# Kernel optimization log

Hardware: AMD Instinct MI355X
Metric: run time of the kernel (lower is better)

Reference implementation:

```python
import jax, jax.numpy as jnp
import numpy as np

EMB = 768
HEADS = 8
HEAD_DIM = EMB // HEADS  # 96
SCALING = HEAD_DIM ** -0.5


def setup_inputs() -> dict:
    key = jax.random.key(0)
    ks = jax.random.split(key, 9)
    B, S = 2, 2048
    std = 1.0 / np.sqrt(EMB)
    x = jax.random.normal(ks[0], (B, S, EMB), dtype=jnp.float32)
    # torch nn.Linear weights are [out, in]; we store [in, out] for x @ W.
    Wq = jax.random.normal(ks[1], (EMB, EMB), dtype=jnp.float32) * std
    Wk = jax.random.normal(ks[2], (EMB, EMB), dtype=jnp.float32) * std
    Wv = jax.random.normal(ks[3], (EMB, EMB), dtype=jnp.float32) * std
    Wo = jax.random.normal(ks[4], (EMB, EMB), dtype=jnp.float32) * std
    bq = jax.random.normal(ks[5], (EMB,), dtype=jnp.float32) * std
    bk = jax.random.normal(ks[6], (EMB,), dtype=jnp.float32) * std
    bv = jax.random.normal(ks[7], (EMB,), dtype=jnp.float32) * std
    bo = jax.random.normal(ks[8], (EMB,), dtype=jnp.float32) * std
    return {"x": x, "Wq": Wq, "bq": bq, "Wk": Wk, "bk": bk,
            "Wv": Wv, "bv": bv, "Wo": Wo, "bo": bo}


def _split_heads(t):
    # [B, S, E] -> [B, H, S, D]
    B, S, _ = t.shape
    return t.reshape(B, S, HEADS, HEAD_DIM).transpose(0, 2, 1, 3)


def reference(x, Wq, bq, Wk, bk, Wv, bv, Wo, bo):
    q = _split_heads(x @ Wq + bq)
    k = _split_heads(x @ Wk + bk)
    v = _split_heads(x @ Wv + bv)
    # Full [B, H, S, S] score matrix, as in the source module.
    energies = jnp.einsum('bhqd,bhkd->bhqk', q, k)
    # Faithful quirk: softmax first, THEN multiply by scaling (dropout=0 -> identity).
    attention = jax.nn.softmax(energies, axis=-1) * SCALING
    out = jnp.einsum('bhqk,bhkd->bhqd', attention, v)
    B, H, S, D = out.shape
    out = out.transpose(0, 2, 1, 3).reshape(B, S, H * D)
    return out @ Wo + bo
```

## Files before the change

### kernel.cpp

```cpp
#include <hip/hip_runtime.h>
#include <hip/hip_bf16.h>

#define EMB 768
#define HD 96
#define NH 8
#define SEQ 2048
#define SCALING 0.10206207261596575f

typedef short bf16x8 __attribute__((ext_vector_type(8)));
typedef float f32x4  __attribute__((ext_vector_type(4)));
typedef unsigned short u16v8 __attribute__((ext_vector_type(8)));
typedef unsigned short u16v4 __attribute__((ext_vector_type(4)));

union F4 { float4 v; float f[4]; };

__device__ __forceinline__ unsigned short f2bf(float v) {
    __hip_bfloat16 b = __float2bfloat16(v);
    return *reinterpret_cast<unsigned short*>(&b);
}
__device__ __forceinline__ float bf2f(unsigned short u) {
    __hip_bfloat16 b = *reinterpret_cast<__hip_bfloat16*>(&u);
    return __bfloat162float(b);
}

__device__ __forceinline__ void dma16(const unsigned short* g, unsigned short* l) {
    __builtin_amdgcn_global_load_lds(
        (const __attribute__((address_space(1))) unsigned int*)g,
        (__attribute__((address_space(3))) unsigned int*)l,
        16, 0, 0);
}

__global__ __launch_bounds__(256) void convert_x(
    const float* __restrict__ x,
    unsigned short* __restrict__ xh, unsigned short* __restrict__ xl)
{
    const size_t i0 = ((size_t)blockIdx.x * 256 + threadIdx.x) * 8;
    F4 a, b;
    a.v = *(const float4*)&x[i0];
    b.v = *(const float4*)&x[i0 + 4];
    u16v8 h, l;
    #pragma unroll
    for (int j = 0; j < 4; j++) {
        unsigned short hu = f2bf(a.f[j]);
        h[j] = hu; l[j] = f2bf(a.f[j] - bf2f(hu));
    }
    #pragma unroll
    for (int j = 0; j < 4; j++) {
        unsigned short hu = f2bf(b.f[j]);
        h[4+j] = hu; l[4+j] = f2bf(b.f[j] - bf2f(hu));
    }
    *(u16v8*)&xh[i0] = h;
    *(u16v8*)&xl[i0] = l;
}

__global__ __launch_bounds__(256) void convert_wT(
    const float* __restrict__ Wq, const float* __restrict__ Wk,
    const float* __restrict__ Wv, const float* __restrict__ Wo,
    unsigned short* __restrict__ WhT, unsigned short* __restrict__ WlT)
{
    const int z = blockIdx.z;
    const float* W = (z == 0) ? Wq : (z == 1) ? Wk : (z == 2) ? Wv : Wo;
    unsigned short* oh = WhT + (size_t)z * 589824;
    unsigned short* ol = WlT + (size_t)z * 589824;
    __shared__ float T[64][68];
    const int t = threadIdx.x;
    const int r = t >> 2, cg = (t & 3) * 16;
    const int k0 = blockIdx.x * 64, n0 = blockIdx.y * 64;
    #pragma unroll
    for (int i = 0; i < 4; i++) {
        float4 v = *(const float4*)&W[(size_t)(k0 + r) * EMB + n0 + cg + 4*i];
        *(float4*)&T[r][cg + 4*i] = v;
    }
    __syncthreads();
    #pragma unroll
    for (int i = 0; i < 4; i++) {
        u16v4 h, l;
        #pragma unroll
        for (int j = 0; j < 4; j++) {
            float v = T[cg + 4*i + j][r];
            unsigned short hu = f2bf(v);
            h[j] = hu; l[j] = f2bf(v - bf2f(hu));
        }
        *(u16v4*)&oh[(size_t)(n0 + r) * EMB + k0 + cg + 4*i] = h;
        *(u16v4*)&ol[(size_t)(n0 + r) * EMB + k0 + cg + 4*i] = l;
    }
}

#define QA_H 0
#define QA_L 4096
#define QW_H 8192
#define QW_L 12288

__global__ __launch_bounds__(256, 3) void qkv_mfma(
    const unsigned short* __restrict__ xh, const unsigned short* __restrict__ xl,
    const unsigned short* __restrict__ WhT, const unsigned short* __restrict__ WlT,
    const float* __restrict__ bq, const float* __restrict__ bk, const float* __restrict__ bv,
    unsigned short* __restrict__ Qh, unsigned short* __restrict__ Ql,
    unsigned short* __restrict__ Kb, unsigned short* __restrict__ Vt)
{
    const int which = blockIdx.z;
    const unsigned short* Wh = WhT + (size_t)which * 589824;
    const unsigned short* Wl = WlT + (size_t)which * 589824;
    const float* bias = (which == 0) ? bq : (which == 1) ? bk : bv;

    __shared__ __align__(16) unsigned short lds[16384];
    const int tid = threadIdx.x;
    const int lane = tid & 63, lo = lane & 15, h4 = lane >> 4;
    const int w = tid >> 6, wm = w & 1, wn = w >> 1;
    const int row0 = blockIdx.x * 128, col0 = blockIdx.y * 128;

    const unsigned short* sbase =
        (w == 0) ? xh + (size_t)row0 * EMB :
        (w == 1) ? xl + (size_t)row0 * EMB :
        (w == 2) ? Wh + (size_t)col0 * EMB :
                   Wl + (size_t)col0 * EMB;
    const int soff = w * 4096;

    f32x4 acc[4][4];
    #pragma unroll
    for (int i = 0; i < 4; i++)
        #pragma unroll
        for (int j = 0; j < 4; j++) acc[i][j] = (f32x4){0.f, 0.f, 0.f, 0.f};

    for (int k0 = 0; k0 < EMB; k0 += 32) {
        #pragma unroll
        for (int j = 0; j < 8; j++) {
            const int u = j*64 + lane;
            const int row = u >> 2, c8 = (u & 3) * 8;
            dma16(sbase + (size_t)row * EMB + k0 + c8, &lds[soff + j*512]);
        }
        __syncthreads();

        bf16x8 ah[4], al[4];
        #pragma unroll
        for (int i = 0; i < 4; i++)
            ah[i] = *(const bf16x8*)&lds[QA_H + (64*wm + 16*i + lo)*32 + 8*h4];
        if (which <= 1) {
            #pragma unroll
            for (int i = 0; i < 4; i++)
                al[i] = *(const bf16x8*)&lds[QA_L + (64*wm + 16*i + lo)*32 + 8*h4];
        }
        #pragma unroll
        for (int j = 0; j < 4; j++) {
            bf16x8 whf = *(const bf16x8*)&lds[QW_H + (64*wn + 16*j + lo)*32 + 8*h4];
            #pragma unroll
            for (int i = 0; i < 4; i++)
                acc[i][j] = __builtin_amdgcn_mfma_f32_16x16x32_bf16(ah[i], whf, acc[i][j], 0, 0, 0);
            if (which <= 1) {
                #pragma unroll
                for (int i = 0; i < 4; i++)
                    acc[i][j] = __builtin_amdgcn_mfma_f32_16x16x32_bf16(al[i], whf, acc[i][j], 0, 0, 0);
            }
            if (which != 1) {
                bf16x8 wlf = *(const bf16x8*)&lds[QW_L + (64*wn + 16*j + lo)*32 + 8*h4];
                #pragma unroll
                for (int i = 0; i < 4; i++)
                    acc[i][j] = __builtin_amdgcn_mfma_f32_16x16x32_bf16(ah[i], wlf, acc[i][j], 0, 0, 0);
            }
        }
        __syncthreads();
    }

    if (which == 0) {
        #pragma unroll
        for (int i = 0; i < 4; i++)
            #pragma unroll
            for (int r = 0; r < 4; r++) {
                const int sg = row0 + 64*wm + 16*i + 4*h4 + r;
                const int b = sg >> 11, s = sg & 2047;
                #pragma unroll
                for (int j = 0; j < 4; j++) {
                    const int c = col0 + 64*wn + 16*j + lo;
                    const int h = c / HD, d = c - h*HD;
                    float v = acc[i][j][r] + bias[c];
                    unsigned short hu = f2bf(v);
                    const size_t base = ((size_t)(b*NH + h) * SEQ + s) * HD + d;
                    Qh[base] = hu;
                    Ql[base] = f2bf(v - bf2f(hu));
                }
            }
    } else if (which == 1) {
        #pragma unroll
        for (int i = 0; i < 4; i++)
            #pragma unroll
            for (int r = 0; r < 4; r++) {
                const int sg = row0 + 64*wm + 16*i + 4*h4 + r;
                const int b = sg >> 11, s = sg & 2047;
                #pragma unroll
                for (int j = 0; j < 4; j++) {
                    const int c = col0 + 64*wn + 16*j + lo;
                    const int h = c / HD, d = c - h*HD;
                    float v = acc[i][j][r] + bias[c];
                    Kb[((size_t)(b*NH + h) * SEQ + s) * HD + d] = f2bf(v);
                }
            }
    } else {
        #pragma unroll
        for (int i = 0; i < 4; i++)
            #pragma unroll
            for (int r = 0; r < 4; r++) {
                const int sg = row0 + 64*wm + 16*i + 4*h4 + r;
                const int b = sg >> 11, s = sg & 2047;
                #pragma unroll
                for (int j = 0; j < 4; j++) {
                    const int c = col0 + 64*wn + 16*j + lo;
                    const int h = c / HD, d = c - h*HD;
                    float v = acc[i][j][r] + bias[c];
                    Vt[((size_t)(b*NH + h) * HD + d) * SEQ + s] = f2bf(v);
                }
            }
    }
}

#define PA_O 0
#define PWH_O 4096
#define PWL_O 6144

__global__ __launch_bounds__(256, 3) void proj_mfma(
    const unsigned short* __restrict__ AOh,
    const unsigned short* __restrict__ Wh, const unsigned short* __restrict__ Wl,
    const float* __restrict__ bo, float* __restrict__ out)
{
    __shared__ __align__(16) unsigned short lds[8192];
    const int tid = threadIdx.x;
    const int lane = tid & 63, lo = lane & 15, h4 = lane >> 4;
    const int w = tid >> 6, wm = w & 1, wn = w >> 1;
    const int row0 = blockIdx.x * 128, col0 = blockIdx.y * 64;

    const unsigned short* sbase =
        (w <= 1) ? AOh + (size_t)row0 * EMB :
        (w == 2) ? Wh  + (size_t)col0 * EMB :
                   Wl  + (size_t)col0 * EMB;
    const int jbase = (w == 1) ? 4 : 0;
    const int soff  = (w <= 1) ? PA_O : (w == 2) ? PWH_O : PWL_O;

    f32x4 acc[4][2];
    #pragma unroll
    for (int i = 0; i < 4; i++)
        #pragma unroll
        for (int j = 0; j < 2; j++) acc[i][j] = (f32x4){0.f, 0.f, 0.f, 0.f};

    for (int k0 = 0; k0 < EMB; k0 += 32) {
        #pragma unroll
        for (int jj = 0; jj < 4; jj++) {
            const int j = jbase + jj;
            const int u = j*64 + lane;
            const int row = u >> 2, c8 = (u & 3) * 8;
            dma16(sbase + (size_t)row * EMB + k0 + c8, &lds[soff + j*512]);
        }
        __syncthreads();

        bf16x8 af[4];
        #pragma unroll
        for (int i = 0; i < 4; i++)
            af[i] = *(const bf16x8*)&lds[PA_O + (64*wm + 16*i + lo)*32 + 8*h4];
        #pragma unroll
        for (int j = 0; j < 2; j++) {
            bf16x8 whf = *(const bf16x8*)&lds[PWH_O + (32*wn + 16*j + lo)*32 + 8*h4];
            bf16x8 wlf = *(const bf16x8*)&lds[PWL_O + (32*wn + 16*j + lo)*32 + 8*h4];
            #pragma unroll
            for (int i = 0; i < 4; i++) {
                acc[i][j] = __builtin_amdgcn_mfma_f32_16x16x32_bf16(af[i], whf, acc[i][j], 0, 0, 0);
                acc[i][j] = __builtin_amdgcn_mfma_f32_16x16x32_bf16(af[i], wlf, acc[i][j], 0, 0, 0);
            }
        }
        __syncthreads();
    }

    #pragma unroll
    for (int i = 0; i < 4; i++)
        #pragma unroll
        for (int r = 0; r < 4; r++) {
            const int sg = row0 + 64*wm + 16*i + 4*h4 + r;
            #pragma unroll
            for (int j = 0; j < 2; j++) {
                const int c = col0 + 32*wn + 16*j + lo;
                out[(size_t)sg * EMB + c] = acc[i][j][r] + bo[c];
            }
        }
}

#define ACH 13568
#define APAIR 27136
#define AP_OFF 54272

__global__ __launch_bounds__(512, 2) void attn_mfma(
    const unsigned short* __restrict__ Qh, const unsigned short* __restrict__ Ql,
    const unsigned short* __restrict__ Kb, const unsigned short* __restrict__ Vt,
    unsigned short* __restrict__ AOh)
{
    __shared__ __align__(16) unsigned short lds[72704];
    const int id   = blockIdx.x;
    const int xcd  = id & 7;
    const int j    = id >> 3;
    const int bh   = 2*xcd + (j & 1);
    const int q0   = (j >> 1) * 128;
    const int tid  = threadIdx.x;
    const int w    = tid >> 6;
    const int g    = w >> 2;
    const int wq   = w & 3;
    const int lane = tid & 63;
    const int lo   = lane & 15;
    const int h4   = lane >> 4;

    const unsigned short* KbH = Kb + (size_t)bh * SEQ * HD;
    const unsigned short* VtH = Vt + (size_t)bh * HD * SEQ;

    const unsigned short* sp0[6];
    int fK[6];
    int doff[6];
    #pragma unroll
    for (int r = 0; r < 6; r++) {
        const int e  = tid + 512*r;
        const int ch = (e >= 1536) ? 1 : 0;
        const int e2 = e - ch*1536;
        if (e2 < 768) {
            const int kk = e2 / 12, g8 = e2 - kk*12;
            sp0[r]  = KbH + (size_t)(ch*64 + kk) * HD + 8*g8;
            fK[r]   = HD;
            doff[r] = ch*ACH + kk*104 + 8*g8;
        } else {
            const int uv = e2 - 768, dV = uv >> 3, c8 = uv & 7;
            sp0[r]  = VtH + (size_t)dV*SEQ + ch*64 + 8*c8;
            fK[r]   = 1;
            doff[r] = ch*ACH + 6656 + dV*72 + 8*c8;
        }
    }

    bf16x8 qhf[2][3], qlf[2][3];
    #pragma unroll
    for (int mi = 0; mi < 2; mi++) {
        const size_t qoff = ((size_t)bh*SEQ + q0 + 32*wq + 16*mi + lo) * HD + 8*h4;
        #pragma unroll
        for (int ks = 0; ks < 3; ks++) {
            qhf[mi][ks] = *(const bf16x8*)&Qh[qoff + 32*ks];
            qlf[mi][ks] = *(const bf16x8*)&Ql[qoff + 32*ks];
        }
    }

    f32x4 O[2][6];
    #pragma unroll
    for (int mi = 0; mi < 2; mi++)
        #pragma unroll
        for (int i = 0; i < 6; i++) O[mi][i] = (f32x4){0.f, 0.f, 0.f, 0.f};
    float lsum[2][4] = {};

    unsigned short* Pw = lds + AP_OFF + w * 2304;

    #pragma unroll
    for (int r = 0; r < 6; r++)
        *(u16v8*)&lds[doff[r]] = *(const u16v8*)sp0[r];
    __syncthreads();

    #pragma unroll 1
    for (int u = 0; u < 16; u++) {
        const int kn0 = (u < 15) ? 128*(u + 1) : 0;
        u16v8 st[6];
        #pragma unroll
        for (int r = 0; r < 6; r++)
            st[r] = *(const u16v8*)(sp0[r] + (size_t)kn0 * fK[r]);

        const unsigned short* myK = lds + (u & 1)*APAIR + g*ACH;
        const unsigned short* myV = myK + 6656;

        f32x4 S[2][4];
        #pragma unroll
        for (int mi = 0; mi < 2; mi++)
            #pragma unroll
            for (int nb = 0; nb < 4; nb++) S[mi][nb] = (f32x4){0.f, 0.f, 0.f, 0.f};
        #pragma unroll
        for (int ks = 0; ks < 3; ks++) {
            bf16x8 kf[4];
            #pragma unroll
            for (int nb = 0; nb < 4; nb++)
                kf[nb] = *(const bf16x8*)&myK[(16*nb + lo)*104 + 32*ks + 8*h4];
            #pragma unroll
            for (int nb = 0; nb < 4; nb++)
                #pragma unroll
                for (int mi = 0; mi < 2; mi++) {
                    S[mi][nb] = __builtin_amdgcn_mfma_f32_16x16x32_bf16(qhf[mi][ks], kf[nb], S[mi][nb], 0, 0, 0);
                    S[mi][nb] = __builtin_amdgcn_mfma_f32_16x16x32_bf16(qlf[mi][ks], kf[nb], S[mi][nb], 0, 0, 0);
                }
        }

        #pragma unroll
        for (int mi = 0; mi < 2; mi++)
            #pragma unroll
            for (int nb = 0; nb < 4; nb++)
                #pragma unroll
                for (int r = 0; r < 4; r++) {
                    float p = __expf(S[mi][nb][r]);
                    lsum[mi][r] += p;
                    Pw[(16*mi + 4*h4 + r)*72 + 16*nb + lo] = f2bf(p);
                }

        #pragma unroll
        for (int ks2 = 0; ks2 < 2; ks2++) {
            bf16x8 pf0 = *(const bf16x8*)&Pw[(lo)*72      + 32*ks2 + 8*h4];
            bf16x8 pf1 = *(const bf16x8*)&Pw[(16 + lo)*72 + 32*ks2 + 8*h4];
            #pragma unroll
            for (int nb2 = 0; nb2 < 6; nb2++) {
                bf16x8 vfv = *(const bf16x8*)&myV[(16*nb2 + lo)*72 + 32*ks2 + 8*h4];
                O[0][nb2] = __builtin_amdgcn_mfma_f32_16x16x32_bf16(pf0, vfv, O[0][nb2], 0, 0, 0);
                O[1][nb2] = __builtin_amdgcn_mfma_f32_16x16x32_bf16(pf1, vfv, O[1][nb2], 0, 0, 0);
            }
        }

        unsigned short* dstp = lds + ((u + 1) & 1)*APAIR;
        #pragma unroll
        for (int r = 0; r < 6; r++)
            *(u16v8*)&dstp[doff[r]] = st[r];
        __syncthreads();
    }

    float* Fo = (float*)lds;
    float* Ls = (float*)lds + 12288;
    if (g == 1) {
        #pragma unroll
        for (int mi = 0; mi < 2; mi++)
            #pragma unroll
            for (int r = 0; r < 4; r++) {
                const int ql = 32*wq + 16*mi + 4*h4 + r;
                Ls[ql*16 + lo] = lsum[mi][r];
                #pragma unroll
                for (int nb2 = 0; nb2 < 6; nb2++)
                    Fo[ql*96 + 16*nb2 + lo] = O[mi][nb2][r];
            }
    }
    __syncthreads();
    if (g == 0) {
        const int b = bh >> 3, hh = bh & 7;
        #pragma unroll
        for (int mi = 0; mi < 2; mi++)
            #pragma unroll
            for (int r = 0; r < 4; r++) {
                const int ql = 32*wq + 16*mi + 4*h4 + r;
                float l = lsum[mi][r] + Ls[ql*16 + lo];
                l += __shfl_xor(l, 1);
                l += __shfl_xor(l, 2);
                l += __shfl_xor(l, 4);
                l += __shfl_xor(l, 8);
                const float sc = SCALING / l;
                const int q = q0 + ql;
                const size_t base = ((size_t)b*SEQ + q)*EMB + hh*HD + lo;
                #pragma unroll
                for (int nb2 = 0; nb2 < 6; nb2++)
                    AOh[base + 16*nb2] = f2bf((O[mi][nb2][r] + Fo[ql*96 + 16*nb2 + lo]) * sc);
            }
    }
}

extern "C" void kernel_launch(void* const* d_in, const int* in_sizes, int n_in,
                              void* d_out, int out_size, void* d_ws, size_t ws_size,
                              hipStream_t stream)
{
    const float* x  = (const float*)d_in[0];
    const float* Wq = (const float*)d_in[1];
    const float* bq = (const float*)d_in[2];
    const float* Wk = (const float*)d_in[3];
    const float* bk = (const float*)d_in[4];
    const float* Wv = (const float*)d_in[5];
    const float* bv = (const float*)d_in[6];
    const float* Wo = (const float*)d_in[7];
    const float* bo = (const float*)d_in[8];
    float* out = (float*)d_out;

    unsigned short* ws = (unsigned short*)d_ws;
    const size_t HS = (size_t)16 * SEQ * HD;
    const size_t WS1 = (size_t)EMB * EMB;
    unsigned short* Qh  = ws;
    unsigned short* Ql  = ws + HS;
    unsigned short* Kb  = ws + 2*HS;
    unsigned short* Vt  = ws + 3*HS;
    unsigned short* xh  = ws + 4*HS;
    unsigned short* xl  = ws + 5*HS;
    unsigned short* WhT = ws + 6*HS;
    unsigned short* WlT = ws + 6*HS + 4*WS1;
    unsigned short* AOh = xh;

    convert_x<<<1536, 256, 0, stream>>>(x, xh, xl);
    convert_wT<<<dim3(12, 12, 4), 256, 0, stream>>>(Wq, Wk, Wv, Wo, WhT, WlT);
    qkv_mfma<<<dim3(32, 6, 3), 256, 0, stream>>>(xh, xl, WhT, WlT, bq, bk, bv,
                                                 Qh, Ql, Kb, Vt);
    attn_mfma<<<256, 512, 0, stream>>>(Qh, Ql, Kb, Vt, AOh);
    proj_mfma<<<dim3(32, 12), 256, 0, stream>>>(AOh, WhT + 3*WS1, WlT + 3*WS1, bo, out);
}
```

Measured before the change: 206.0 us.

## Merge conversion kernels, shrink projection tiles, prioritize MFMA waves in attention

After: 204.1 us. Within noise of the previous version (-0.9%).

```diff
diff --git a/kernel.cpp b/kernel.cpp
--- a/kernel.cpp
+++ b/kernel.cpp
@@ -30,59 +30,61 @@
         16, 0, 0);
 }
 
-__global__ __launch_bounds__(256) void convert_x(
+__global__ __launch_bounds__(256) void convert_all(
     const float* __restrict__ x,
-    unsigned short* __restrict__ xh, unsigned short* __restrict__ xl)
-{
-    const size_t i0 = ((size_t)blockIdx.x * 256 + threadIdx.x) * 8;
-    F4 a, b;
-    a.v = *(const float4*)&x[i0];
-    b.v = *(const float4*)&x[i0 + 4];
-    u16v8 h, l;
-    #pragma unroll
-    for (int j = 0; j < 4; j++) {
-        unsigned short hu = f2bf(a.f[j]);
-        h[j] = hu; l[j] = f2bf(a.f[j] - bf2f(hu));
-    }
-    #pragma unroll
-    for (int j = 0; j < 4; j++) {
-        unsigned short hu = f2bf(b.f[j]);
-        h[4+j] = hu; l[4+j] = f2bf(b.f[j] - bf2f(hu));
-    }
-    *(u16v8*)&xh[i0] = h;
-    *(u16v8*)&xl[i0] = l;
-}
-
-__global__ __launch_bounds__(256) void convert_wT(
     const float* __restrict__ Wq, const float* __restrict__ Wk,
     const float* __restrict__ Wv, const float* __restrict__ Wo,
+    unsigned short* __restrict__ xh, unsigned short* __restrict__ xl,
     unsigned short* __restrict__ WhT, unsigned short* __restrict__ WlT)
 {
-    const int z = blockIdx.z;
-    const float* W = (z == 0) ? Wq : (z == 1) ? Wk : (z == 2) ? Wv : Wo;
-    unsigned short* oh = WhT + (size_t)z * 589824;
-    unsigned short* ol = WlT + (size_t)z * 589824;
     __shared__ float T[64][68];
-    const int t = threadIdx.x;
-    const int r = t >> 2, cg = (t & 3) * 16;
-    const int k0 = blockIdx.x * 64, n0 = blockIdx.y * 64;
-    #pragma unroll
-    for (int i = 0; i < 4; i++) {
-        float4 v = *(const float4*)&W[(size_t)(k0 + r) * EMB + n0 + cg + 4*i];
-        *(float4*)&T[r][cg + 4*i] = v;
-    }
-    __syncthreads();
-    #pragma unroll
-    for (int i = 0; i < 4; i++) {
-        u16v4 h, l;
+    if (blockIdx.x < 1536) {
+        const size_t i0 = ((size_t)blockIdx.x * 256 + threadIdx.x) * 8;
+        F4 a, b;
+        a.v = *(const float4*)&x[i0];
+        b.v = *(const float4*)&x[i0 + 4];
+        u16v8 h, l;
         #pragma unroll
         for (int j = 0; j < 4; j++) {
-            float v = T[cg + 4*i + j][r];
-            unsigned short hu = f2bf(v);
-            h[j] = hu; l[j] = f2bf(v - bf2f(hu));
-        }
-        *(u16v4*)&oh[(size_t)(n0 + r) * EMB + k0 + cg + 4*i] = h;
-        *(u16v4*)&ol[(size_t)(n0 + r) * EMB + k0 + cg + 4*i] = l;
+            unsigned short hu = f2bf(a.f[j]);
+            h[j] = hu; l[j] = f2bf(a.f[j] - bf2f(hu));
+        }
+        #pragma unroll
+        for (int j = 0; j < 4; j++) {
+            unsigned short hu = f2bf(b.f[j]);
+            h[4+j] = hu; l[4+j] = f2bf(b.f[j] - bf2f(hu));
+        }
+        *(u16v8*)&xh[i0] = h;
+        *(u16v8*)&xl[i0] = l;
+    } else {
+        const int tb = blockIdx.x - 1536;
+        const int z  = tb / 144;
+        const int r2 = tb - z*144;
+        const int bx = r2 / 12, by = r2 - bx*12;
+        const float* W = (z == 0) ? Wq : (z == 1) ? Wk : (z == 2) ? Wv : Wo;
+        unsigned short* oh = WhT + (size_t)z * 589824;
+        unsigned short* ol = WlT + (size_t)z * 589824;
+        const int t = threadIdx.x;
+        const int r = t >> 2, cg = (t & 3) * 16;
+        const int k0 = bx * 64, n0 = by * 64;
+        #pragma unroll
+        for (int i = 0; i < 4; i++) {
+            float4 v = *(const float4*)&W[(size_t)(k0 + r) * EMB + n0 + cg + 4*i];
+            *(float4*)&T[r][cg + 4*i] = v;
+        }
+        __syncthreads();
+        #pragma unroll
+        for (int i = 0; i < 4; i++) {
+            u16v4 h, l;
+            #pragma unroll
+            for (int j = 0; j < 4; j++) {
+                float v = T[cg + 4*i + j][r];
+                unsigned short hu = f2bf(v);
+                h[j] = hu; l[j] = f2bf(v - bf2f(hu));
+            }
+            *(u16v4*)&oh[(size_t)(n0 + r) * EMB + k0 + cg + 4*i] = h;
+            *(u16v4*)&ol[(size_t)(n0 + r) * EMB + k0 + cg + 4*i] = l;
+        }
     }
 }
 
@@ -213,53 +215,49 @@
 }
 
 #define PA_O 0
-#define PWH_O 4096
-#define PWL_O 6144
+#define PWH_O 2048
+#define PWL_O 4096
 
 __global__ __launch_bounds__(256, 3) void proj_mfma(
     const unsigned short* __restrict__ AOh,
     const unsigned short* __restrict__ Wh, const unsigned short* __restrict__ Wl,
     const float* __restrict__ bo, float* __restrict__ out)
 {
-    __shared__ __align__(16) unsigned short lds[8192];
+    __shared__ __align__(16) unsigned short lds[6144];
     const int tid = threadIdx.x;
     const int lane = tid & 63, lo = lane & 15, h4 = lane >> 4;
     const int w = tid >> 6, wm = w & 1, wn = w >> 1;
-    const int row0 = blockIdx.x * 128, col0 = blockIdx.y * 64;
-
-    const unsigned short* sbase =
-        (w <= 1) ? AOh + (size_t)row0 * EMB :
-        (w == 2) ? Wh  + (size_t)col0 * EMB :
-                   Wl  + (size_t)col0 * EMB;
-    const int jbase = (w == 1) ? 4 : 0;
-    const int soff  = (w <= 1) ? PA_O : (w == 2) ? PWH_O : PWL_O;
-
-    f32x4 acc[4][2];
-    #pragma unroll
-    for (int i = 0; i < 4; i++)
+    const int row0 = blockIdx.x * 64, col0 = blockIdx.y * 64;
+    const int r16 = lane >> 2, c8 = (lane & 3) * 8;
+
+    f32x4 acc[2][2];
+    #pragma unroll
+    for (int i = 0; i < 2; i++)
         #pragma unroll
         for (int j = 0; j < 2; j++) acc[i][j] = (f32x4){0.f, 0.f, 0.f, 0.f};
 
     for (int k0 = 0; k0 < EMB; k0 += 32) {
         #pragma unroll
-        for (int jj = 0; jj < 4; jj++) {
-            const int j = jbase + jj;
-            const int u = j*64 + lane;
-            const int row = u >> 2, c8 = (u & 3) * 8;
-            dma16(sbase + (size_t)row * EMB + k0 + c8, &lds[soff + j*512]);
-        }
-        __syncthreads();
-
-        bf16x8 af[4];
-        #pragma unroll
-        for (int i = 0; i < 4; i++)
-            af[i] = *(const bf16x8*)&lds[PA_O + (64*wm + 16*i + lo)*32 + 8*h4];
+        for (int jj = 0; jj < 3; jj++) {
+            const int u = w*3 + jj;
+            const unsigned short* g; int ld;
+            if (u < 4)      { g = AOh + (size_t)(row0 + u*16     + r16) * EMB + k0 + c8; ld = PA_O  + u*512; }
+            else if (u < 8) { g = Wh  + (size_t)(col0 + (u-4)*16 + r16) * EMB + k0 + c8; ld = PWH_O + (u-4)*512; }
+            else            { g = Wl  + (size_t)(col0 + (u-8)*16 + r16) * EMB + k0 + c8; ld = PWL_O + (u-8)*512; }
+            dma16(g, &lds[ld]);
+        }
+        __syncthreads();
+
+        bf16x8 af[2];
+        #pragma unroll
+        for (int i = 0; i < 2; i++)
+            af[i] = *(const bf16x8*)&lds[PA_O + (32*wm + 16*i + lo)*32 + 8*h4];
         #pragma unroll
         for (int j = 0; j < 2; j++) {
             bf16x8 whf = *(const bf16x8*)&lds[PWH_O + (32*wn + 16*j + lo)*32 + 8*h4];
             bf16x8 wlf = *(const bf16x8*)&lds[PWL_O + (32*wn + 16*j + lo)*32 + 8*h4];
             #pragma unroll
-            for (int i = 0; i < 4; i++) {
+            for (int i = 0; i < 2; i++) {
                 acc[i][j] = __builtin_amdgcn_mfma_f32_16x16x32_bf16(af[i], whf, acc[i][j], 0, 0, 0);
                 acc[i][j] = __builtin_amdgcn_mfma_f32_16x16x32_bf16(af[i], wlf, acc[i][j], 0, 0, 0);
             }
@@ -268,10 +266,10 @@
     }
 
     #pragma unroll
-    for (int i = 0; i < 4; i++)
+    for (int i = 0; i < 2; i++)
         #pragma unroll
         for (int r = 0; r < 4; r++) {
-            const int sg = row0 + 64*wm + 16*i + 4*h4 + r;
+            const int sg = row0 + 32*wm + 16*i + 4*h4 + r;
             #pragma unroll
             for (int j = 0; j < 2; j++) {
                 const int c = col0 + 32*wn + 16*j + lo;
@@ -368,6 +366,7 @@
         for (int mi = 0; mi < 2; mi++)
             #pragma unroll
             for (int nb = 0; nb < 4; nb++) S[mi][nb] = (f32x4){0.f, 0.f, 0.f, 0.f};
+        __builtin_amdgcn_s_setprio(1);
         #pragma unroll
         for (int ks = 0; ks < 3; ks++) {
             bf16x8 kf[4];
@@ -382,6 +381,7 @@
                     S[mi][nb] = __builtin_amdgcn_mfma_f32_16x16x32_bf16(qlf[mi][ks], kf[nb], S[mi][nb], 0, 0, 0);
                 }
         }
+        __builtin_amdgcn_s_setprio(0);
 
         #pragma unroll
         for (int mi = 0; mi < 2; mi++)
@@ -394,6 +394,7 @@
                     Pw[(16*mi + 4*h4 + r)*72 + 16*nb + lo] = f2bf(p);
                 }
 
+        __builtin_amdgcn_s_setprio(1);
         #pragma unroll
         for (int ks2 = 0; ks2 < 2; ks2++) {
             bf16x8 pf0 = *(const bf16x8*)&Pw[(lo)*72      + 32*ks2 + 8*h4];
@@ -405,6 +406,7 @@
                 O[1][nb2] = __builtin_amdgcn_mfma_f32_16x16x32_bf16(pf1, vfv, O[1][nb2], 0, 0, 0);
             }
         }
+        __builtin_amdgcn_s_setprio(0);
 
         unsigned short* dstp = lds + ((u + 1) & 1)*APAIR;
         #pragma unroll
@@ -478,10 +480,9 @@
     unsigned short* WlT = ws + 6*HS + 4*WS1;
     unsigned short* AOh = xh;
 
-    convert_x<<<1536, 256, 0, stream>>>(x, xh, xl);
-    convert_wT<<<dim3(12, 12, 4), 256, 0, stream>>>(Wq, Wk, Wv, Wo, WhT, WlT);
+    convert_all<<<2112, 256, 0, stream>>>(x, Wq, Wk, Wv, Wo, xh, xl, WhT, WlT);
     qkv_mfma<<<dim3(32, 6, 3), 256, 0, stream>>>(xh, xl, WhT, WlT, bq, bk, bv,
                                                  Qh, Ql, Kb, Vt);
     attn_mfma<<<256, 512, 0, stream>>>(Qh, Ql, Kb, Vt, AOh);
-    proj_mfma<<<dim3(32, 12), 256, 0, stream>>>(AOh, WhT + 3*WS1, WlT + 3*WS1, bo, out);
-}
+    proj_mfma<<<dim3(64, 12), 256, 0, stream>>>(AOh, WhT + 3*WS1, WlT + 3*WS1, bo, out);
+}
```
